# Optimization experiments

Hardware: AMD Instinct MI355X
Metric: run time of the kernel (lower is better)

Reference implementation:

```python
import jax, jax.numpy as jnp
import numpy as np
from jax import lax

BBOX_XFORM_CLIP = float(np.log(1000.0 / 16.0))
PRE_NMS_TOP_K = 1000
SCORE_THRESH = 0.05
IOU_THRESH = 0.5
MAX_DET = 100


def _decode_boxes(encoded, anchors):
    # encoded [...,4] = [dy,dx,dh,dw] with weights [10,10,5,5]; anchors [...,4] = [y1,x1,y2,x2]
    dy = encoded[..., 0] / 10.0
    dx = encoded[..., 1] / 10.0
    dh = jnp.minimum(encoded[..., 2] / 5.0, BBOX_XFORM_CLIP)
    dw = jnp.minimum(encoded[..., 3] / 5.0, BBOX_XFORM_CLIP)
    ah = anchors[..., 2] - anchors[..., 0]
    aw = anchors[..., 3] - anchors[..., 1]
    ayc = anchors[..., 0] + 0.5 * ah
    axc = anchors[..., 1] + 0.5 * aw
    yc = dy * ah + ayc
    xc = dx * aw + axc
    h = jnp.exp(dh) * ah
    w = jnp.exp(dw) * aw
    return jnp.stack([yc - 0.5 * h, xc - 0.5 * w, yc + 0.5 * h, xc + 0.5 * w], axis=-1)


def _clip_boxes(boxes, image_shape):
    # boxes [B,N,4]; image_shape [B,2] = (height, width)
    h = image_shape[..., 0:1]
    w = image_shape[..., 1:2]
    maxlen = jnp.concatenate([h, w, h, w], axis=-1)[:, None, :]  # [B,1,4]
    return jnp.clip(boxes, 0.0, maxlen)


def _nms_keep(boxes):
    # Greedy sequential NMS on score-sorted boxes [k,4]; returns keep mask [k].
    k = boxes.shape[0]
    y1, x1, y2, x2 = boxes[:, 0], boxes[:, 1], boxes[:, 2], boxes[:, 3]
    area = (y2 - y1) * (x2 - x1)
    idxs = jnp.arange(k)

    def body(keep, i):
        iy1 = jnp.maximum(y1[i], y1)
        ix1 = jnp.maximum(x1[i], x1)
        iy2 = jnp.minimum(y2[i], y2)
        ix2 = jnp.minimum(x2[i], x2)
        inter = jnp.maximum(iy2 - iy1, 0.0) * jnp.maximum(ix2 - ix1, 0.0)
        union = area[i] + area - inter
        iou = inter / jnp.where(union > 0, union, 1.0)
        suppressed = jnp.any(keep & (idxs < i) & (iou > IOU_THRESH))
        return keep.at[i].set(~suppressed), None

    keep, _ = lax.scan(body, jnp.zeros((k,), jnp.bool_), idxs)
    return keep


def _nms_single(boxes, scores):
    # boxes [k,4], scores [k] sorted descending; mirrors sorted_non_max_suppression_padded output.
    keep = _nms_keep(lax.stop_gradient(boxes))
    valid = keep & jnp.any(boxes > 0, axis=-1)  # zeroed (filtered) boxes never count
    sel = jnp.where(valid, scores, -jnp.inf)
    top_s, top_i = lax.top_k(sel, MAX_DET)
    out_valid = top_s > -jnp.inf
    out_scores = jnp.where(out_valid, top_s, 0.0)
    out_boxes = boxes[top_i] * out_valid[:, None].astype(boxes.dtype)
    return out_scores, out_boxes


def setup_inputs() -> dict:
    key = jax.random.key(0)
    k1, k2, k3, k4 = jax.random.split(key, 4)
    B, K, C = 8, 8192, 91
    raw_boxes = jax.random.normal(k1, (B, K, C * 4), jnp.float32) * 0.5
    raw_scores = jax.random.normal(k2, (B, K, C), jnp.float32) * 2.0
    # valid anchors [y1,x1,y2,x2] inside a 1024x1024 image
    ctr = jax.random.uniform(k3, (B, K, 2), jnp.float32, 0.0, 1024.0)
    sz = jax.random.uniform(k4, (B, K, 2), jnp.float32, 16.0, 128.0)
    anchor_boxes = jnp.concatenate([ctr - 0.5 * sz, ctr + 0.5 * sz], axis=-1)
    image_shape = jnp.full((B, 2), 1024.0, jnp.float32)
    return {"raw_boxes": raw_boxes, "raw_scores": raw_scores,
            "anchor_boxes": anchor_boxes, "image_shape": image_shape}


def reference(raw_boxes, raw_scores, anchor_boxes, image_shape):
    B, K, C = raw_scores.shape
    Cc = C - 1  # background removed

    probs = jax.nn.softmax(raw_scores, axis=-1)[:, :, 1:]           # [B,K,Cc]
    boxes = raw_boxes.reshape(B, K, C, 4)[:, :, 1:, :]              # [B,K,Cc,4]
    anch = jnp.broadcast_to(anchor_boxes[:, :, None, :], boxes.shape)
    dec = _decode_boxes(boxes.reshape(B, K * Cc, 4), anch.reshape(B, K * Cc, 4))
    dec = _clip_boxes(dec, image_shape).reshape(B, K, Cc, 4)

    # per-class top-k pre-NMS candidates (_select_top_k_scores + gather)
    k = min(K, PRE_NMS_TOP_K)
    s_t = jnp.transpose(probs, (0, 2, 1))                           # [B,Cc,K]
    top_s, top_i = lax.top_k(s_t, k)                                # [B,Cc,k]
    b_t = jnp.transpose(dec, (0, 2, 1, 3))                          # [B,Cc,K,4]
    top_b = jnp.take_along_axis(b_t, top_i[..., None], axis=2)      # [B,Cc,k,4]

    # filter_boxes_by_scores: score -> -1, box -> 0 below threshold
    mask = top_s > SCORE_THRESH
    top_s = jnp.where(mask, top_s, -1.0)
    top_b = top_b * mask[..., None].astype(top_b.dtype)

    nms_s, nms_b = jax.vmap(jax.vmap(_nms_single))(top_b, top_s)    # [B,Cc,MAX_DET], [B,Cc,MAX_DET,4]
    classes = jnp.broadcast_to(jnp.arange(Cc, dtype=jnp.int32)[None, :, None], nms_s.shape)

    all_s = nms_s.reshape(B, Cc * MAX_DET)
    all_b = nms_b.reshape(B, Cc * MAX_DET, 4)
    all_c = classes.reshape(B, Cc * MAX_DET)

    fin_s, fin_i = lax.top_k(all_s, MAX_DET)
    fin_b = jnp.take_along_axis(all_b, fin_i[..., None], axis=1)
    fin_c = jnp.take_along_axis(all_c, fin_i, axis=1) + 1           # restore background offset
    num = jnp.sum((fin_s > -1.0).astype(jnp.int32), axis=1)
    return fin_b, fin_s, fin_c, num
```

## Files before the change

kernel.cpp:

```cpp
#include <hip/hip_runtime.h>
#include <stdint.h>

typedef unsigned long long ull;

#define K_ANCH   8192
#define NCLS     91
#define NCC      90
#define B_SZ     8
#define CAP      1024
#define PRE_NMS  1000
#define MAXDET   100
#define CHUNK    64
#define NWMAX    16
#define NBW      128
#define SCORE_TH 0.05f
#define IOU_TH   0.5f
#define BBOX_CLIP 4.1351665565490723f

__device__ __forceinline__ float wave_max64(float v) {
  #pragma unroll
  for (int off = 32; off > 0; off >>= 1) v = fmaxf(v, __shfl_xor(v, off, 64));
  return v;
}
__device__ __forceinline__ float wave_sum64(float v) {
  #pragma unroll
  for (int off = 32; off > 0; off >>= 1) v += __shfl_xor(v, off, 64);
  return v;
}

__device__ __forceinline__ float4 decode_clip(float4 e, float4 a, float imh, float imw) {
#pragma clang fp contract(off)
  float dy = e.x / 10.0f;
  float dx = e.y / 10.0f;
  float dh = fminf(e.z / 5.0f, BBOX_CLIP);
  float dw = fminf(e.w / 5.0f, BBOX_CLIP);
  float ah = a.z - a.x;
  float aw = a.w - a.y;
  float ayc = a.x + 0.5f * ah;
  float axc = a.y + 0.5f * aw;
  float yc = dy * ah + ayc;
  float xc = dx * aw + axc;
  float h = expf(dh) * ah;
  float w = expf(dw) * aw;
  float y1 = yc - 0.5f * h, x1 = xc - 0.5f * w;
  float y2 = yc + 0.5f * h, x2 = xc + 0.5f * w;
  y1 = fminf(fmaxf(y1, 0.0f), imh);
  x1 = fminf(fmaxf(x1, 0.0f), imw);
  y2 = fminf(fmaxf(y2, 0.0f), imh);
  x2 = fminf(fmaxf(x2, 0.0f), imw);
  return make_float4(y1, x1, y2, x2);
}

__device__ __forceinline__ bool iou_gt(float4 bi, float ai, float4 bj, float aj) {
#pragma clang fp contract(off)
  float iy1 = fmaxf(bi.x, bj.x);
  float ix1 = fmaxf(bi.y, bj.y);
  float iy2 = fminf(bi.z, bj.z);
  float ix2 = fminf(bi.w, bj.w);
  float inter = fmaxf(iy2 - iy1, 0.0f) * fmaxf(ix2 - ix1, 0.0f);
  float uni = ai + aj - inter;
  float iou = inter / (uni > 0.0f ? uni : 1.0f);
  return iou > IOU_TH;
}

__global__ __launch_bounds__(1024) void kT_softmax(
    const float* __restrict__ raw_scores, const float* __restrict__ raw_boxes,
    const float4* __restrict__ anchors, const float* __restrict__ image_shape,
    float2* __restrict__ stats, ull* __restrict__ bmask,
    float* __restrict__ pstage, float4* __restrict__ bstage, int pcap)
{
  __shared__ ull    rowbits[64][2];
  __shared__ float  sp[64][92];
  __shared__ float4 sanch[64];
  __shared__ int    wl[5760];
  __shared__ int    wl_n;
  int tid = threadIdx.x;
  int wv = tid >> 6, lane = tid & 63;
  int b = blockIdx.x >> 7;
  int k0 = (blockIdx.x & 127) << 6;
  if (tid == 0) wl_n = 0;
  if (tid < 64) sanch[tid] = anchors[(size_t)b * K_ANCH + k0 + tid];
  #pragma unroll
  for (int i = 0; i < 4; i++) {
    int rl = (wv << 2) + i;
    int row = b * K_ANCH + k0 + rl;
    const float* srow = raw_scores + (size_t)row * NCLS;
    float s0 = srow[lane];
    bool has1 = lane < (NCLS - 64);
    float s1 = has1 ? srow[64 + lane] : -INFINITY;
    float m = wave_max64(fmaxf(s0, s1));
    float e0 = expf(s0 - m);
    float e1 = has1 ? expf(s1 - m) : 0.0f;
    float denom = wave_sum64(e0 + e1);
    float p0 = e0 / denom;
    float p1 = e1 / denom;
    sp[rl][lane] = p0;
    if (has1) sp[rl][64 + lane] = p1;
    ull b0 = __ballot(lane >= 1 && p0 > SCORE_TH);
    ull b1 = __ballot(has1 && p1 > SCORE_TH);
    if (lane == 0) {
      stats[row] = make_float2(m, denom);
      rowbits[rl][0] = b0;
      rowbits[rl][1] = b1;
    }
  }
  __syncthreads();
  if (tid < NCC) {
    int c = tid + 1, w = c >> 6, bit = c & 63;
    ull out = 0;
    #pragma unroll
    for (int r = 0; r < 64; r++)
      out |= ((rowbits[r][w] >> bit) & 1ull) << r;
    bmask[(size_t)(b * NCC + tid) * NBW + (k0 >> 6)] = out;
    int cnt = __popcll(out);
    if (cnt > 0) {
      int basei = atomicAdd(&wl_n, cnt);
      ull m = out;
      int rank = 0;
      while (m) {
        int r = __ffsll(m) - 1;
        m &= m - 1;
        wl[basei + rank] = (c << 12) | (r << 6) | rank;
        rank++;
      }
    }
  }
  __syncthreads();
  int nwl = wl_n;
  if (pcap > 0) {
    float imh = image_shape[b * 2 + 0];
    float imw = image_shape[b * 2 + 1];
    for (int t = tid; t < nwl; t += 1024) {
      int e = wl[t];
      int c = e >> 12, r = (e >> 6) & 63, rank = e & 63;
      if (rank >= pcap) continue;
      size_t row = (size_t)b * K_ANCH + k0 + r;
      float4 enc = ((const float4*)raw_boxes)[row * NCLS + c];
      float4 box = decode_clip(enc, sanch[r], imh, imw);
      size_t pw = (size_t)(b * NCC + (c - 1)) * NBW + (k0 >> 6);
      pstage[pw * pcap + rank] = sp[r][c];
      bstage[pw * pcap + rank] = box;
    }
  }
}

__global__ __launch_bounds__(256) void kN_nms(
    const float* __restrict__ raw_boxes, const float* __restrict__ raw_scores,
    const float4* __restrict__ anchors, const float* __restrict__ image_shape,
    const float2* __restrict__ stats, const ull* __restrict__ bmask,
    const float* __restrict__ pstage, const float4* __restrict__ bstage, int pcap,
    float* __restrict__ all_s, float4* __restrict__ all_b)
{
  __shared__ float4 sbox[PRE_NMS];
  __shared__ float  sarea[PRE_NMS];
  __shared__ float  sscore[PRE_NMS];
  __shared__ ull    sbuf[1056];
  __shared__ ull    sbm[NBW];
  __shared__ int    soff[NBW];
  __shared__ int    swtot[2];
  __shared__ int    s_n;
  __shared__ int    s_done;
#define SMASK(w, r) sbuf[(w) * (CHUNK + 1) + (r)]

  int bc  = blockIdx.x;
  int tid = threadIdx.x;
  int b = bc / NCC;
  int c = bc - b * NCC + 1;
  int outbase = bc * MAXDET;
  size_t rowb = (size_t)b * K_ANCH;

  for (int i = tid; i < MAXDET; i += 256) {
    all_s[outbase + i] = 0.0f;
    all_b[outbase + i] = make_float4(0.f, 0.f, 0.f, 0.f);
  }

  ull w0 = 0;
  int cnt = 0;
  if (tid < NBW) {
    w0 = bmask[(size_t)bc * NBW + tid];
    sbm[tid] = w0;
    cnt = __popcll(w0);
  }
  int incl = cnt;
  if (tid < 128) {
    int lane = tid & 63;
    #pragma unroll
    for (int d = 1; d < 64; d <<= 1) {
      int o = __shfl_up(incl, d, 64);
      if (lane >= d) incl += o;
    }
    if (lane == 63) swtot[tid >> 6] = incl;
  }
  if (tid == 0) s_done = 0;
  __syncthreads();
  if (tid < 128) soff[tid] = incl - cnt + ((tid >= 64) ? swtot[0] : 0);
  if (tid == 0) s_n = swtot[0] + swtot[1];
  __syncthreads();
  int n_load = min(s_n, CAP);

  if (tid < NBW) {
    int slot = soff[tid];
    ull m = w0;
    int kb = tid << 6;
    int rank = 0;
    size_t pw = (size_t)bc * NBW + tid;
    while (m) {
      int bit = __ffsll(m) - 1;
      m &= m - 1;
      int k = kb + bit;
      float p;
      if (rank < pcap) {
        p = pstage[pw * (size_t)pcap + rank];
      } else {
        size_t row = rowb + k;
        float s = raw_scores[row * NCLS + c];
        float2 md = stats[row];
        p = expf(s - md.x) / md.y;
      }
      if (slot < CAP)
        sbuf[slot] = ((ull)__float_as_uint(p) << 32) | (uint32_t)(K_ANCH - 1 - k);
      slot++;
      rank++;
    }
  }
  int n2 = (n_load <= 512) ? 512 : 1024;
  for (int i = n_load + tid; i < n2; i += 256) sbuf[i] = 0ull;
  __syncthreads();

  if (n_load <= 512) {
    ull e0 = sbuf[tid], e1 = sbuf[tid + 256];
    for (int size = 2; size <= 512; size <<= 1) {
      if (size == 512 && e0 < e1) { ull t = e0; e0 = e1; e1 = t; }
      for (int s = ((size >> 1) > 128 ? 128 : (size >> 1)); s >= 64; s >>= 1) {
        __syncthreads();
        sbuf[tid] = e0; sbuf[tid + 256] = e1;
        __syncthreads();
        ull p0 = sbuf[tid ^ s];
        ull p1 = sbuf[(tid + 256) ^ s];
        bool t0 = (((tid & s) == 0) == ((tid & size) == 0));
        bool t1 = ((((tid + 256) & s) == 0) == (((tid + 256) & size) == 0));
        e0 = t0 ? (e0 > p0 ? e0 : p0) : (e0 < p0 ? e0 : p0);
        e1 = t1 ? (e1 > p1 ? e1 : p1) : (e1 < p1 ? e1 : p1);
      }
      int smax = ((size >> 1) < 32 ? (size >> 1) : 32);
      for (int s = smax; s >= 1; s >>= 1) {
        ull p0 = __shfl_xor(e0, s, 64);
        ull p1 = __shfl_xor(e1, s, 64);
        bool t0 = (((tid & s) == 0) == ((tid & size) == 0));
        bool t1 = ((((tid + 256) & s) == 0) == (((tid + 256) & size) == 0));
        e0 = t0 ? (e0 > p0 ? e0 : p0) : (e0 < p0 ? e0 : p0);
        e1 = t1 ? (e1 > p1 ? e1 : p1) : (e1 < p1 ? e1 : p1);
      }
    }
    __syncthreads();
    sbuf[tid] = e0;
    sbuf[tid + 256] = e1;
    __syncthreads();
  } else {
    for (int size = 2; size <= 1024; size <<= 1) {
      for (int stride = size >> 1; stride > 0; stride >>= 1) {
        for (int i = tid; i < 1024; i += 256) {
          int j = i ^ stride;
          if (j > i) {
            ull ki = sbuf[i], kj = sbuf[j];
            bool desc = ((i & size) == 0);
            if (desc ? (ki < kj) : (ki > kj)) { sbuf[i] = kj; sbuf[j] = ki; }
          }
        }
        __syncthreads();
      }
    }
  }

  int n_use = min(n_load, PRE_NMS);
  float imh = image_shape[b * 2 + 0];
  float imw = image_shape[b * 2 + 1];
  for (int i = tid; i < n_use; i += 256) {
    ull key = sbuf[i];
    int k = K_ANCH - 1 - (int)(key & 0xFFFFFFFFull);
    int w = k >> 6;
    int rank = __popcll(sbm[w] & ((1ull << (k & 63)) - 1ull));
    float4 box;
    if (rank < pcap) {
      box = bstage[((size_t)bc * NBW + w) * (size_t)pcap + rank];
    } else {
      size_t row = rowb + k;
      float4 e = ((const float4*)raw_boxes)[row * NCLS + c];
      box = decode_clip(e, anchors[row], imh, imw);
    }
    sbox[i] = box;
    sscore[i] = __uint_as_float((uint32_t)(key >> 32));
    {
#pragma clang fp contract(off)
      sarea[i] = (box.z - box.x) * (box.w - box.y);
    }
  }

  int nwords = (n_use + 63) >> 6;
  ull rem = 0;
  int written = 0;
  for (int c0 = 0; c0 < n_use; c0 += CHUNK) {
    __syncthreads();
    if (s_done) break;
    int nrows = min(CHUNK, n_use - c0);

    for (int p = tid; p < (nwords << 6); p += 256) {
      int w  = p >> 6;
      int rr = p & (CHUNK - 1);
      if (rr >= nrows) continue;
      int r = c0 + rr;
      float4 br = sbox[r];
      float  ar = sarea[r];
      int j0 = w << 6;
      int j1 = min(j0 + 64, n_use);
      int js = max(j0, r + 1);
      ull mrow = 0;
      for (int j = js; j < j1; j++) {
        if (iou_gt(br, ar, sbox[j], sarea[j])) mrow |= 1ull << (j - j0);
      }
      SMASK(w, rr) = mrow;
    }
    __syncthreads();

    if (tid < 64) {
      int lane = tid;
      for (int i = c0; i < c0 + nrows; i++) {
        int w = i >> 6, bit = i & 63;
        ull rw = __shfl(rem, w, 64);
        if (((rw >> bit) & 1ull) == 0) {
          if (lane < nwords) rem |= SMASK(lane, i - c0);
          int valid = 0;
          float4 bx;
          float sc = 0.f;
          if (lane == 0) {
            bx = sbox[i];
            valid = (bx.x > 0.f || bx.y > 0.f || bx.z > 0.f || bx.w > 0.f) ? 1 : 0;
            sc = sscore[i];
          }
          valid = __shfl(valid, 0, 64);
          if (valid) {
            if (lane == 0) {
              all_s[outbase + written] = sc;
              all_b[outbase + written] = bx;
            }
            written++;
            if (written == MAXDET) {
              if (lane == 0) s_done = 1;
              break;
            }
          }
        }
      }
    }
  }
#undef SMASK
}

__global__ __launch_bounds__(256) void k3_final(
    const float* __restrict__ all_s, const float4* __restrict__ all_b,
    float* __restrict__ out)
{
  __shared__ float ss[NCC * MAXDET];
  int b = blockIdx.x;
  int tid = threadIdx.x;
  const float* S = all_s + (size_t)b * NCC * MAXDET;
  for (int i = tid; i < NCC * MAXDET; i += 256) ss[i] = S[i];
  __syncthreads();
  if (tid >= 64) return;
  int lane = tid;

  float* fin_b = out;
  float* fin_s = out + B_SZ * MAXDET * 4;
  float* fin_c = fin_s + B_SZ * MAXDET;
  float* numo  = fin_c + B_SZ * MAXDET;

  int c0 = lane;
  int c1 = lane + 64;
  int p0 = 0, p1 = 0;
  ull cur0 = ((ull)__float_as_uint(ss[c0 * MAXDET]) << 32) | (uint32_t)(16383 - c0 * MAXDET);
  ull nxt0 = ((ull)__float_as_uint(ss[c0 * MAXDET + 1]) << 32) | (uint32_t)(16383 - (c0 * MAXDET + 1));
  ull cur1 = 0ull, nxt1 = 0ull;
  if (c1 < NCC) {
    cur1 = ((ull)__float_as_uint(ss[c1 * MAXDET]) << 32) | (uint32_t)(16383 - c1 * MAXDET);
    nxt1 = ((ull)__float_as_uint(ss[c1 * MAXDET + 1]) << 32) | (uint32_t)(16383 - (c1 * MAXDET + 1));
  }
  int cnt = 0;

  for (int step = 0; step < MAXDET; step++) {
    ull my = (cur0 > cur1) ? cur0 : cur1;
    ull g = my;
    #pragma unroll
    for (int off = 32; off > 0; off >>= 1) {
      ull o = __shfl_xor(g, off, 64);
      g = (o > g) ? o : g;
    }
    if (cur0 != 0ull && g == cur0) {
      p0++;
      cur0 = nxt0;
      int f = c0 * MAXDET + p0 + 1;
      nxt0 = (p0 + 1 < MAXDET)
           ? (((ull)__float_as_uint(ss[f]) << 32) | (uint32_t)(16383 - f)) : 0ull;
    } else if (cur1 != 0ull && g == cur1) {
      p1++;
      cur1 = nxt1;
      int f = c1 * MAXDET + p1 + 1;
      nxt1 = (p1 + 1 < MAXDET)
           ? (((ull)__float_as_uint(ss[f]) << 32) | (uint32_t)(16383 - f)) : 0ull;
    }

    if (lane == 0) {
      int flat = 16383 - (int)(g & 0xFFFFFFFFull);
      int cc = flat / MAXDET;
      float sc = __uint_as_float((uint32_t)(g >> 32));
      fin_s[b * MAXDET + step] = sc;
      fin_c[b * MAXDET + step] = (float)(cc + 1);
      float4 bx = all_b[(size_t)b * NCC * MAXDET + flat];
      ((float4*)fin_b)[b * MAXDET + step] = bx;
      if (sc > -1.0f) cnt++;
    }
  }
  if (lane == 0) numo[b] = (float)cnt;
}

extern "C" void kernel_launch(void* const* d_in, const int* in_sizes, int n_in,
                              void* d_out, int out_size, void* d_ws, size_t ws_size,
                              hipStream_t stream) {
  const float*  raw_boxes   = (const float*)d_in[0];
  const float*  raw_scores  = (const float*)d_in[1];
  const float4* anchors     = (const float4*)d_in[2];
  const float*  image_shape = (const float*)d_in[3];

  char* p = (char*)d_ws;
  size_t used = 0;
  auto alloc = [&](size_t bytes) {
    char* r = p + used;
    used += (bytes + 255) & ~(size_t)255;
    return r;
  };
  float2* stats = (float2*)alloc((size_t)B_SZ * K_ANCH * sizeof(float2));
  ull*    bmask = (ull*)   alloc((size_t)B_SZ * NCC * NBW * sizeof(ull));
  float*  all_s = (float*) alloc((size_t)B_SZ * NCC * MAXDET * sizeof(float));
  float4* all_b = (float4*)alloc((size_t)B_SZ * NCC * MAXDET * sizeof(float4));

  size_t nw = (size_t)B_SZ * NCC * NBW;
  int pcap = 16;
  while (pcap > 0 && used + ((nw * pcap * 4 + 255) & ~(size_t)255)
                          + ((nw * pcap * 16 + 255) & ~(size_t)255) > ws_size)
    pcap >>= 1;
  float*  pstage = (float*) alloc(nw * (size_t)pcap * 4);
  float4* bstage = (float4*)alloc(nw * (size_t)pcap * 16);

  kT_softmax<<<B_SZ * 128, 1024, 0, stream>>>(raw_scores, raw_boxes, anchors, image_shape,
                                              stats, bmask, pstage, bstage, pcap);
  kN_nms<<<B_SZ * NCC, 256, 0, stream>>>(raw_boxes, raw_scores, anchors, image_shape,
                                         stats, bmask, pstage, bstage, pcap, all_s, all_b);
  k3_final<<<B_SZ, 256, 0, stream>>>(all_s, all_b, (float*)d_out);
}
```

Before: 311.8 us.

## Restructure bitmask NMS to compute IoU only for kept rows per column tile

Replaces the row-chunked NMS, which built the full upper-triangular suppression mask against all column words, with a column-tile loop. For each 64-box column tile, IoU masks are computed only for rows already kept in earlier tiles plus rows in the current tile. A wave then ORs the kept rows' masks to get the incoming suppression and resolves the tile greedily with shuffles. This skips IoU work for suppressed boxes and shortens the serial resolve loop. In exchange, each tile adds a block-wide reduction over prior rows and two syncs.

```diff
diff --git a/kernel.cpp b/kernel.cpp
--- a/kernel.cpp
+++ b/kernel.cpp
@@ -10,7 +10,6 @@
 #define CAP      1024
 #define PRE_NMS  1000
 #define MAXDET   100
-#define CHUNK    64
 #define NWMAX    16
 #define NBW      128
 #define SCORE_TH 0.05f
@@ -156,11 +155,11 @@
   __shared__ float  sscore[PRE_NMS];
   __shared__ ull    sbuf[1056];
   __shared__ ull    sbm[NBW];
+  __shared__ ull    skw[NWMAX];
   __shared__ int    soff[NBW];
   __shared__ int    swtot[2];
   __shared__ int    s_n;
   __shared__ int    s_done;
-#define SMASK(w, r) sbuf[(w) * (CHUNK + 1) + (r)]
 
   int bc  = blockIdx.x;
   int tid = threadIdx.x;
@@ -173,6 +172,7 @@
     all_s[outbase + i] = 0.0f;
     all_b[outbase + i] = make_float4(0.f, 0.f, 0.f, 0.f);
   }
+  if (tid < NWMAX) skw[tid] = 0ull;
 
   ull w0 = 0;
   int cnt = 0;
@@ -296,52 +296,56 @@
     }
   }
 
-  int nwords = (n_use + 63) >> 6;
-  ull rem = 0;
+  int nwords_use = (n_use + 63) >> 6;
   int written = 0;
-  for (int c0 = 0; c0 < n_use; c0 += CHUNK) {
+  for (int t = 0; t < nwords_use; t++) {
     __syncthreads();
     if (s_done) break;
-    int nrows = min(CHUNK, n_use - c0);
-
-    for (int p = tid; p < (nwords << 6); p += 256) {
-      int w  = p >> 6;
-      int rr = p & (CHUNK - 1);
-      if (rr >= nrows) continue;
-      int r = c0 + rr;
-      float4 br = sbox[r];
-      float  ar = sarea[r];
-      int j0 = w << 6;
-      int j1 = min(j0 + 64, n_use);
-      int js = max(j0, r + 1);
+    int j0 = t << 6;
+    int j1 = min(j0 + 64, n_use);
+    int r_lim = j1;
+
+    for (int r = tid; r < r_lim; r += 256) {
+      bool need = (r >= j0) || ((skw[r >> 6] >> (r & 63)) & 1ull);
       ull mrow = 0;
-      for (int j = js; j < j1; j++) {
-        if (iou_gt(br, ar, sbox[j], sarea[j])) mrow |= 1ull << (j - j0);
-      }
-      SMASK(w, rr) = mrow;
+      if (need) {
+        float4 br = sbox[r];
+        float  ar = sarea[r];
+        int js = max(j0, r + 1);
+        for (int j = js; j < j1; j++)
+          if (iou_gt(br, ar, sbox[j], sarea[j])) mrow |= 1ull << (j - j0);
+      }
+      sbuf[r] = mrow;
     }
     __syncthreads();
 
     if (tid < 64) {
       int lane = tid;
-      for (int i = c0; i < c0 + nrows; i++) {
-        int w = i >> 6, bit = i & 63;
-        ull rw = __shfl(rem, w, 64);
-        if (((rw >> bit) & 1ull) == 0) {
-          if (lane < nwords) rem |= SMASK(lane, i - c0);
-          int valid = 0;
-          float4 bx;
-          float sc = 0.f;
-          if (lane == 0) {
-            bx = sbox[i];
-            valid = (bx.x > 0.f || bx.y > 0.f || bx.z > 0.f || bx.w > 0.f) ? 1 : 0;
-            sc = sscore[i];
-          }
-          valid = __shfl(valid, 0, 64);
-          if (valid) {
+      ull acc = 0;
+      for (int r = lane; r < j0; r += 64)
+        if ((skw[r >> 6] >> (r & 63)) & 1ull) acc |= sbuf[r];
+      #pragma unroll
+      for (int off = 32; off > 0; off >>= 1) acc |= __shfl_xor(acc, off, 64);
+      ull supp = acc;
+      ull mj = (j0 + lane < n_use) ? sbuf[j0 + lane] : 0ull;
+      bool vj = false;
+      float4 bl;
+      if (j0 + lane < n_use) {
+        bl = sbox[j0 + lane];
+        vj = (bl.x > 0.f || bl.y > 0.f || bl.z > 0.f || bl.w > 0.f);
+      }
+      ull vball = __ballot(vj);
+      ull keptw = 0;
+      int nrows = j1 - j0;
+      for (int j = 0; j < nrows; j++) {
+        if (!((supp >> j) & 1ull)) {
+          keptw |= 1ull << j;
+          supp |= __shfl(mj, j, 64);
+          if ((vball >> j) & 1ull) {
             if (lane == 0) {
-              all_s[outbase + written] = sc;
-              all_b[outbase + written] = bx;
+              int i = j0 + j;
+              all_s[outbase + written] = sscore[i];
+              all_b[outbase + written] = sbox[i];
             }
             written++;
             if (written == MAXDET) {
@@ -351,9 +355,9 @@
           }
         }
       }
-    }
-  }
-#undef SMASK
+      if (lane == 0) skw[t] = keptw;
+    }
+  }
 }
 
 __global__ __launch_bounds__(256) void k3_final(
```

Result: faster. 277.5 us (-11.0%).
